# Kernel optimization log

Measured on AMD Instinct MI355X. Metric: run time of the kernel, lower is better.

The kernel has to match this reference:

```python
import jax, jax.numpy as jnp
import numpy as np

N = 10000      # nodes
E = 160000     # edges (before self-loops)
H = 2          # ATTN_HEADS
D_IN = 256
C1 = 256       # hidden_channels per head in conv1
C2 = 512       # per-head channels in conv2 (hardcoded 512 in module)
OUT = 3


def setup_inputs():
    key = jax.random.key(0)
    ks = jax.random.split(key, 20)
    rn = lambda k, s, sc=0.05: jax.random.normal(k, s, jnp.float32) * sc
    return {
        "x": jax.random.normal(ks[0], (N, D_IN), jnp.float32),
        "edge_index": jax.random.randint(ks[1], (2, E), 0, N),
        # conv1: lin_src/lin_dst [D_IN, H*C1], attention vecs [H, C1], bias [H*C1]
        "w1s": rn(ks[2], (D_IN, H * C1)), "w1d": rn(ks[3], (D_IN, H * C1)),
        "a1s": rn(ks[4], (H, C1)), "a1d": rn(ks[5], (H, C1)), "b1": rn(ks[6], (H * C1,)),
        # conv2: input dim H*C1 -> [H*C1, H*C2]
        "w2s": rn(ks[7], (H * C1, H * C2)), "w2d": rn(ks[8], (H * C1, H * C2)),
        "a2s": rn(ks[9], (H, C2)), "a2d": rn(ks[10], (H, C2)), "b2": rn(ks[11], (H * C2,)),
        # MLP head
        "wf1": rn(ks[12], (H * C2, 128)), "bf1": rn(ks[13], (128,)),
        "gamma": jnp.ones((128,), jnp.float32), "beta": jnp.zeros((128,), jnp.float32),
        "wf2": rn(ks[14], (128, OUT)), "bf2": rn(ks[15], (OUT,)),
    }


def gat_layer(x, src, dst, Ws, Wd, att_s, att_d, b, n):
    h, c = att_s.shape
    xs = (x @ Ws).reshape(n, h, c)                      # [N,H,C] source messages
    xd = (x @ Wd).reshape(n, h, c)
    a_s = (xs * att_s).sum(-1)                          # [N,H]
    a_d = (xd * att_d).sum(-1)
    e = a_s[src] + a_d[dst]                             # [E,H]
    e = jnp.where(e > 0, e, 0.2 * e)                    # leaky_relu(0.2)
    m = jax.lax.stop_gradient(jax.ops.segment_max(e, dst, num_segments=n))
    alpha = jnp.exp(e - m[dst])
    denom = jax.ops.segment_sum(alpha, dst, num_segments=n)
    alpha = alpha / denom[dst]                          # segment softmax over dst
    out = jax.ops.segment_sum(xs[src] * alpha[..., None], dst, num_segments=n)
    return out.reshape(n, h * c) + b                    # concat heads + bias


def reference(x, edge_index, w1s, w1d, a1s, a1d, b1, w2s, w2d, a2s, a2d, b2,
              wf1, bf1, gamma, beta, wf2, bf2):
    loops = jnp.arange(N, dtype=edge_index.dtype)
    src = jnp.concatenate([edge_index[0], loops])       # add self-loops (PyG default)
    dst = jnp.concatenate([edge_index[1], loops])
    h = jax.nn.relu(gat_layer(x, src, dst, w1s, w1d, a1s, a1d, b1, N))
    h = jax.nn.relu(gat_layer(h, src, dst, w2s, w2d, a2s, a2d, b2, N))
    h = h @ wf1 + bf1
    mean = h.mean(0)
    var = ((h - mean) ** 2).mean(0)
    h = gamma * (h - mean) * jax.lax.rsqrt(var + 1e-5) + beta
    h = jax.nn.relu(h)
    h = h @ wf2 + bf2
    return jax.nn.log_softmax(h, axis=-1)
```

## Files before the change

kernel.cpp:

```cpp
#include <hip/hip_runtime.h>
#include <cstdint>
#include <cstddef>


typedef unsigned short u16;
typedef __bf16 bf16x8 __attribute__((ext_vector_type(8)));
typedef float f32x4 __attribute__((ext_vector_type(4)));
typedef unsigned short u16x8 __attribute__((ext_vector_type(8)));

__device__ __forceinline__ u16 f2b(float f) {
  union { float f; uint32_t u; } c; c.f = f;
  uint32_t u = c.u;
  return (u16)((u + 0x7FFFu + ((u >> 16) & 1u)) >> 16);
}
__device__ __forceinline__ float b2f(u16 h) {
  union { uint32_t u; float f; } c; c.u = ((uint32_t)h) << 16;
  return c.f;
}

__device__ __forceinline__ void async16(const void* g, void* l) {
  __builtin_amdgcn_global_load_lds((const __attribute__((address_space(1))) void*)g,
                                   (__attribute__((address_space(3))) void*)l, 16, 0, 0);
}

__device__ __forceinline__ float2 edge_w(const float4& as, const float4& ad) {
  float e0 = as.x + ad.z; e0 = e0 > 0.f ? e0 : 0.2f * e0;
  float e1 = as.y + ad.w; e1 = e1 > 0.f ? e1 : 0.2f * e1;
  return make_float2(__expf(e0), __expf(e1));
}

__device__ __forceinline__ void transpose_tile(const float* __restrict__ W, u16* __restrict__ WT,
                                               int K, int NC, int b, int t,
                                               u16 (*tile)[66]) {
  int tn = NC >> 6;
  int ti = b / tn, tj = b - ti * tn;
  int col = t & 63, r0 = t >> 6;
  const float* src = W + (size_t)(ti * 64) * NC + tj * 64;
#pragma unroll
  for (int i = 0; i < 16; i++) {
    int r = r0 + i * 4;
    tile[r][col] = f2b(src[(size_t)r * NC + col]);
  }
  __syncthreads();
  u16* dst = WT + (size_t)(tj * 64) * K + ti * 64;
#pragma unroll
  for (int i = 0; i < 16; i++) {
    int r = r0 + i * 4;
    dst[(size_t)r * K + col] = tile[col][r];
  }
}

__global__ __launch_bounds__(256) void prep(
    const float* __restrict__ x,
    const float* __restrict__ w1s, const float* __restrict__ w1d,
    const float* __restrict__ w2s, const float* __restrict__ w2d,
    const float* __restrict__ wf1,
    const float* __restrict__ a1s, const float* __restrict__ a1d,
    const float* __restrict__ a2s, const float* __restrict__ a2d,
    u16* __restrict__ xb, u16* __restrict__ w1T, u16* __restrict__ w2T,
    u16* __restrict__ wf1T, float* __restrict__ V1, float* __restrict__ V2,
    uint32_t* __restrict__ arena, int arena_nwords, int za,
    uint32_t* __restrict__ g1pad, int g1w, int zg1,
    uint32_t* __restrict__ g2pad, int g2w,
    int N) {
  __shared__ u16 tile[64][66];
  int b = blockIdx.x, t = threadIdx.x;
  const int R0 = 32;
  const int R1 = R0 + 128;
  const int R2 = R1 + 32;
  const int R3 = R2 + 256;
  const int R4 = R3 + 512;
  const int R5 = R4 + N;
  const int R6 = R5 + za;
  const int R7 = R6 + zg1;

  if (b < R0) {
    transpose_tile(w1s, w1T, 256, 512, b, t, tile);
  } else if (b < R1) {
    transpose_tile(w2s, w2T, 512, 1024, b - R0, t, tile);
  } else if (b < R2) {
    transpose_tile(wf1, wf1T, 1024, 128, b - R1, t, tile);
  } else if (b < R3) {
    int wv = t >> 6, lane = t & 63;
    int u = (b - R2) * 4 + wv;
    int k = u >> 2, which = (u >> 1) & 1, h = u & 1;
    const float* W = which ? w1d : w1s;
    const float* att = which ? a1d : a1s;
    float s = 0.f;
#pragma unroll
    for (int c = lane; c < 256; c += 64) s += W[k * 512 + h * 256 + c] * att[h * 256 + c];
#pragma unroll
    for (int o = 32; o > 0; o >>= 1) s += __shfl_down(s, o);
    if (lane == 0) V1[k * 4 + which * 2 + h] = s;
  } else if (b < R4) {
    int wv = t >> 6, lane = t & 63;
    int u = (b - R3) * 4 + wv;
    int k = u >> 2, which = (u >> 1) & 1, h = u & 1;
    const float* W = which ? w2d : w2s;
    const float* att = which ? a2d : a2s;
    float s = 0.f;
#pragma unroll
    for (int c = lane; c < 512; c += 64) s += W[k * 1024 + h * 512 + c] * att[h * 512 + c];
#pragma unroll
    for (int o = 32; o > 0; o >>= 1) s += __shfl_down(s, o);
    if (lane == 0) V2[k * 4 + which * 2 + h] = s;
  } else if (b < R5) {
    int row = b - R4;
    int idx = row * 256 + t;
    xb[idx] = f2b(x[idx]);
  } else if (b < R6) {
    int idx = (b - R5) * 256 + t;
    if (idx < arena_nwords) arena[idx] = 0u;
  } else if (b < R7) {
    int idx = (b - R6) * 256 + t;
    if (idx < g1w) g1pad[idx] = 0u;
  } else {
    int idx = (b - R7) * 256 + t;
    if (idx < g2w) g2pad[idx] = 0u;
  }
}

__global__ __launch_bounds__(256) void fill_a(const int* __restrict__ srcs,
                                              const int* __restrict__ dsts,
                                              int* __restrict__ cursor, int* __restrict__ csr,
                                              const float* __restrict__ X,
                                              const float* __restrict__ V,
                                              float* __restrict__ A, int N, int E, int FB) {
  int b = blockIdx.x, t = threadIdx.x;
  if (b < FB) {
    int i = b * 256 + t;
    if (i < N) {
      csr[(size_t)i * 64] = i;
    } else if (i < N + E) {
      int e = i - N;
      int d = dsts[e];
      int slot = atomicAdd(&cursor[d], 1) + 1;
      if (slot < 64) csr[(size_t)d * 64 + slot] = srcs[e];
    }
    return;
  }
  int node = (b - FB) * 4 + (t >> 6);
  int lane = t & 63;
  if (node >= N) return;
  const float* xr = X + (size_t)node * 256;
  float s0 = 0, s1 = 0, s2 = 0, s3 = 0;
  {
    int k = lane * 4;
    float4 xv = *(const float4*)(xr + k);
    float xe[4] = {xv.x, xv.y, xv.z, xv.w};
#pragma unroll
    for (int j = 0; j < 4; j++) {
      float4 v = ((const float4*)V)[k + j];
      s0 += xe[j] * v.x; s1 += xe[j] * v.y; s2 += xe[j] * v.z; s3 += xe[j] * v.w;
    }
  }
#pragma unroll
  for (int o = 32; o > 0; o >>= 1) {
    s0 += __shfl_down(s0, o); s1 += __shfl_down(s1, o);
    s2 += __shfl_down(s2, o); s3 += __shfl_down(s3, o);
  }
  if (lane == 0) ((float4*)A)[node] = make_float4(s0, s1, s2, s3);
}

__global__ __launch_bounds__(256) void agg1(const u16* __restrict__ xs,
                                            const float* __restrict__ a,
                                            const int* __restrict__ cursor,
                                            const int* __restrict__ csr,
                                            u16* __restrict__ g, int N) {
  int v = blockIdx.x * 8 + (threadIdx.x >> 5);
  if (v >= N) return;
  int c0 = (threadIdx.x & 31) * 8;
  const int* seg = csr + (size_t)v * 64;
  int cnt = min(cursor[v], 63) + 1;
  const float4* a4 = (const float4*)a;
  float4 adv = a4[v];
  float h0[8], h1[8];
#pragma unroll
  for (int j = 0; j < 8; j++) { h0[j] = 0.f; h1[j] = 0.f; }
  float den0 = 0.f, den1 = 0.f;
  int i = 0;
  for (; i + 4 <= cnt; i += 4) {
    int4 s4 = *(const int4*)(seg + i);
    float4 aa0 = a4[s4.x], aa1 = a4[s4.y], aa2 = a4[s4.z], aa3 = a4[s4.w];
    u16x8 x0 = *(const u16x8*)(xs + (size_t)s4.x * 256 + c0);
    u16x8 x1 = *(const u16x8*)(xs + (size_t)s4.y * 256 + c0);
    u16x8 x2 = *(const u16x8*)(xs + (size_t)s4.z * 256 + c0);
    u16x8 x3 = *(const u16x8*)(xs + (size_t)s4.w * 256 + c0);
    float2 w0 = edge_w(aa0, adv), w1 = edge_w(aa1, adv);
    float2 w2 = edge_w(aa2, adv), w3 = edge_w(aa3, adv);
    den0 += w0.x + w1.x + w2.x + w3.x;
    den1 += w0.y + w1.y + w2.y + w3.y;
#pragma unroll
    for (int j = 0; j < 8; j++) {
      float f0 = b2f(x0[j]), f1 = b2f(x1[j]), f2 = b2f(x2[j]), f3 = b2f(x3[j]);
      h0[j] += w0.x * f0 + w1.x * f1 + w2.x * f2 + w3.x * f3;
      h1[j] += w0.y * f0 + w1.y * f1 + w2.y * f2 + w3.y * f3;
    }
  }
  for (; i < cnt; i++) {
    int s = seg[i];
    float2 w = edge_w(a4[s], adv);
    den0 += w.x; den1 += w.y;
    u16x8 xv = *(const u16x8*)(xs + (size_t)s * 256 + c0);
#pragma unroll
    for (int j = 0; j < 8; j++) {
      float f = b2f(xv[j]);
      h0[j] += w.x * f;
      h1[j] += w.y * f;
    }
  }
  float r0 = 1.f / den0, r1 = 1.f / den1;
  u16x8 o0v, o1v;
#pragma unroll
  for (int j = 0; j < 8; j++) {
    o0v[j] = f2b(h0[j] * r0);
    o1v[j] = f2b(h1[j] * r1);
  }
  u16* grow = g + (size_t)v * 512;
  *(u16x8*)(grow + c0) = o0v;
  *(u16x8*)(grow + 256 + c0) = o1v;
}

__global__ __launch_bounds__(256) void agg2(const u16* __restrict__ xs,
                                            const float* __restrict__ a,
                                            const int* __restrict__ cursor,
                                            const int* __restrict__ csr,
                                            u16* __restrict__ g, int N) {
  int v = blockIdx.x * 4 + (threadIdx.x >> 6);
  if (v >= N) return;
  int c0 = (threadIdx.x & 63) * 8;
  const int* seg = csr + (size_t)v * 64;
  int cnt = min(cursor[v], 63) + 1;
  const float4* a4 = (const float4*)a;
  float4 adv = a4[v];
  float h0[8], h1[8];
#pragma unroll
  for (int j = 0; j < 8; j++) { h0[j] = 0.f; h1[j] = 0.f; }
  float den0 = 0.f, den1 = 0.f;
  int i = 0;
  for (; i + 4 <= cnt; i += 4) {
    int4 s4 = *(const int4*)(seg + i);
    float4 aa0 = a4[s4.x], aa1 = a4[s4.y], aa2 = a4[s4.z], aa3 = a4[s4.w];
    u16x8 x0 = *(const u16x8*)(xs + (size_t)s4.x * 512 + c0);
    u16x8 x1 = *(const u16x8*)(xs + (size_t)s4.y * 512 + c0);
    u16x8 x2 = *(const u16x8*)(xs + (size_t)s4.z * 512 + c0);
    u16x8 x3 = *(const u16x8*)(xs + (size_t)s4.w * 512 + c0);
    float2 w0 = edge_w(aa0, adv), w1 = edge_w(aa1, adv);
    float2 w2 = edge_w(aa2, adv), w3 = edge_w(aa3, adv);
    den0 += w0.x + w1.x + w2.x + w3.x;
    den1 += w0.y + w1.y + w2.y + w3.y;
#pragma unroll
    for (int j = 0; j < 8; j++) {
      float f0 = b2f(x0[j]), f1 = b2f(x1[j]), f2 = b2f(x2[j]), f3 = b2f(x3[j]);
      h0[j] += w0.x * f0 + w1.x * f1 + w2.x * f2 + w3.x * f3;
      h1[j] += w0.y * f0 + w1.y * f1 + w2.y * f2 + w3.y * f3;
    }
  }
  for (; i < cnt; i++) {
    int s = seg[i];
    float2 w = edge_w(a4[s], adv);
    den0 += w.x; den1 += w.y;
    u16x8 xv = *(const u16x8*)(xs + (size_t)s * 512 + c0);
#pragma unroll
    for (int j = 0; j < 8; j++) {
      float f = b2f(xv[j]);
      h0[j] += w.x * f;
      h1[j] += w.y * f;
    }
  }
  float r0 = 1.f / den0, r1 = 1.f / den1;
  u16x8 o0v, o1v;
#pragma unroll
  for (int j = 0; j < 8; j++) {
    o0v[j] = f2b(h0[j] * r0);
    o1v[j] = f2b(h1[j] * r1);
  }
  u16* grow = g + (size_t)v * 1024;
  *(u16x8*)(grow + c0) = o0v;
  *(u16x8*)(grow + 512 + c0) = o1v;
}

template <bool OUT_BF16, bool A2OUT>
__global__ __launch_bounds__(256) void gemm_bf16(const u16* __restrict__ A, int lda, int aZ,
                                                 const u16* __restrict__ BT, int ldb, int bZ,
                                                 const float* __restrict__ bias, int biasZ,
                                                 int relu, void* __restrict__ Cv, int ldc,
                                                 size_t cZ, int K, float* __restrict__ a2out,
                                                 const float* __restrict__ Vfold) {
  __shared__ u16 Asl[2][128 * 32];
  __shared__ u16 Bsl[2][128 * 32];
  int tid = threadIdx.x;
  int wave = tid >> 6, lane = tid & 63;
  int wr = wave >> 1, wc = wave & 1;
  int lr = lane & 15, quad = lane >> 4;
  size_t row0 = (size_t)blockIdx.y * 128;
  size_t n0 = (size_t)blockIdx.x * 128;
  int zq = blockIdx.z;
  int k0base = 0;
  if (OUT_BF16) {
    A += (size_t)zq * aZ;
    BT += (size_t)zq * bZ;
    bias += (size_t)zq * biasZ;
  } else {
    k0base = zq * K;
  }

  f32x4 acc[4][4];
#pragma unroll
  for (int i = 0; i < 4; i++)
#pragma unroll
    for (int j = 0; j < 4; j++) acc[i][j] = (f32x4){0.f, 0.f, 0.f, 0.f};

  int ra = tid >> 2;
  int ca = (tid & 3) * 8;
  const u16* gA = A + (row0 + ra) * lda + ca;
  const u16* gB = BT + (n0 + ra) * ldb + ca;
  int lbase = (tid & 192) * 8;

  async16(gA + k0base, &Asl[0][lbase]);
  async16(gA + (size_t)64 * lda + k0base, &Asl[0][lbase + 2048]);
  async16(gB + k0base, &Bsl[0][lbase]);
  async16(gB + (size_t)64 * ldb + k0base, &Bsl[0][lbase + 2048]);
  __syncthreads();

  int nIter = K >> 5;
  for (int it = 0; it < nIter; it++) {
    int cur = it & 1;
    if (it + 1 < nIter) {
      int kn = k0base + (it + 1) * 32;
      async16(gA + kn, &Asl[1 - cur][lbase]);
      async16(gA + (size_t)64 * lda + kn, &Asl[1 - cur][lbase + 2048]);
      async16(gB + kn, &Bsl[1 - cur][lbase]);
      async16(gB + (size_t)64 * ldb + kn, &Bsl[1 - cur][lbase + 2048]);
    }
    bf16x8 av[4], bv[4];
#pragma unroll
    for (int i = 0; i < 4; i++)
      av[i] = *(const bf16x8*)&Asl[cur][(wr * 64 + i * 16 + lr) * 32 + quad * 8];
#pragma unroll
    for (int j = 0; j < 4; j++)
      bv[j] = *(const bf16x8*)&Bsl[cur][(wc * 64 + j * 16 + lr) * 32 + quad * 8];
#pragma unroll
    for (int i = 0; i < 4; i++)
#pragma unroll
      for (int j = 0; j < 4; j++)
        acc[i][j] = __builtin_amdgcn_mfma_f32_16x16x32_bf16(av[i], bv[j], acc[i][j], 0, 0, 0);
    __syncthreads();
  }

  size_t crow = row0 + wr * 64 + quad * 4;
  size_t ccol = n0 + wc * 64 + lr;
  if (OUT_BF16) {
    float bj[4];
#pragma unroll
    for (int j = 0; j < 4; j++) bj[j] = bias[ccol + j * 16];
    float4 vr[4];
    if (A2OUT) {
#pragma unroll
      for (int j = 0; j < 4; j++)
        vr[j] = ((const float4*)Vfold)[(size_t)zq * cZ + ccol + j * 16];
    }
    u16* C = (u16*)Cv + (size_t)zq * cZ;
#pragma unroll
    for (int i = 0; i < 4; i++) {
#pragma unroll
      for (int r = 0; r < 4; r++) {
        float pa0 = 0.f, pa1 = 0.f, pa2 = 0.f, pa3 = 0.f;
#pragma unroll
        for (int j = 0; j < 4; j++) {
          float val = acc[i][j][r] + bj[j];
          if (relu) val = fmaxf(val, 0.f);
          C[(crow + i * 16 + r) * ldc + ccol + j * 16] = f2b(val);
          if (A2OUT) {
            pa0 += val * vr[j].x; pa1 += val * vr[j].y;
            pa2 += val * vr[j].z; pa3 += val * vr[j].w;
          }
        }
        if (A2OUT) {
#pragma unroll
          for (int o = 8; o > 0; o >>= 1) {
            pa0 += __shfl_down(pa0, o); pa1 += __shfl_down(pa1, o);
            pa2 += __shfl_down(pa2, o); pa3 += __shfl_down(pa3, o);
          }
          if (lr == 0) {
            float* ap = a2out + (crow + i * 16 + r) * 4;
            atomicAdd(ap + 0, pa0); atomicAdd(ap + 1, pa1);
            atomicAdd(ap + 2, pa2); atomicAdd(ap + 3, pa3);
          }
        }
      }
    }
  } else {
    float* C = (float*)Cv + (size_t)zq * cZ;
#pragma unroll
    for (int i = 0; i < 4; i++)
#pragma unroll
      for (int j = 0; j < 4; j++)
#pragma unroll
        for (int r = 0; r < 4; r++)
          C[(crow + i * 16 + r) * ldc + ccol + j * 16] = acc[i][j][r];
  }
}

__global__ __launch_bounds__(128) void col_stats(const float* __restrict__ z, size_t slab,
                                                 float* __restrict__ sums, int N) {
  int j = threadIdx.x;
  float s = 0.f, s2 = 0.f;
  for (int n = blockIdx.x; n < N; n += gridDim.x) {
    const float* p = z + (size_t)n * 128 + j;
    float v = p[0] + p[slab] + p[2 * slab] + p[3 * slab];
    s += v; s2 += v * v;
  }
  atomicAdd(&sums[j], s);
  atomicAdd(&sums[128 + j], s2);
}

__global__ __launch_bounds__(256) void head_kernel(const float* __restrict__ z, size_t slab,
                                                   const float* __restrict__ sums,
                                                   const float* __restrict__ gamma,
                                                   const float* __restrict__ beta,
                                                   const float* __restrict__ wf2,
                                                   const float* __restrict__ bf2,
                                                   float* __restrict__ out, int N) {
  int v = blockIdx.x * 4 + (threadIdx.x >> 6);
  if (v >= N) return;
  int lane = threadIdx.x & 63;
  float inv = 1.f / (float)N;
  float p0 = 0.f, p1 = 0.f, p2 = 0.f;
#pragma unroll
  for (int half = 0; half < 2; half++) {
    int j = lane + half * 64;
    float mean = sums[j] * inv;
    float var = sums[128 + j] * inv - mean * mean;
    float rstd = rsqrtf(var + 1e-5f);
    const float* p = z + (size_t)v * 128 + j;
    float h = p[0] + p[slab] + p[2 * slab] + p[3 * slab];
    h = gamma[j] * (h - mean) * rstd + beta[j];
    h = h > 0.f ? h : 0.f;
    p0 += h * wf2[j * 3 + 0];
    p1 += h * wf2[j * 3 + 1];
    p2 += h * wf2[j * 3 + 2];
  }
#pragma unroll
  for (int o = 32; o > 0; o >>= 1) {
    p0 += __shfl_down(p0, o);
    p1 += __shfl_down(p1, o);
    p2 += __shfl_down(p2, o);
  }
  if (lane == 0) {
    float l0 = p0 + bf2[0], l1 = p1 + bf2[1], l2 = p2 + bf2[2];
    float mx = fmaxf(l0, fmaxf(l1, l2));
    float lse = mx + logf(__expf(l0 - mx) + __expf(l1 - mx) + __expf(l2 - mx));
    out[v * 3 + 0] = l0 - lse;
    out[v * 3 + 1] = l1 - lse;
    out[v * 3 + 2] = l2 - lse;
  }
}

extern "C" void kernel_launch(void* const* d_in, const int* in_sizes, int n_in,
                              void* d_out, int out_size, void* d_ws, size_t ws_size,
                              hipStream_t stream) {
  const float* x     = (const float*)d_in[0];
  const int*   ei    = (const int*)d_in[1];
  const float* w1s   = (const float*)d_in[2];
  const float* w1d   = (const float*)d_in[3];
  const float* a1s   = (const float*)d_in[4];
  const float* a1d   = (const float*)d_in[5];
  const float* b1    = (const float*)d_in[6];
  const float* w2s   = (const float*)d_in[7];
  const float* w2d   = (const float*)d_in[8];
  const float* a2s   = (const float*)d_in[9];
  const float* a2d   = (const float*)d_in[10];
  const float* b2    = (const float*)d_in[11];
  const float* wf1   = (const float*)d_in[12];
  const float* gamma = (const float*)d_in[14];
  const float* beta  = (const float*)d_in[15];
  const float* wf2   = (const float*)d_in[16];
  const float* bf2   = (const float*)d_in[17];
  float* out = (float*)d_out;

  const int N = in_sizes[0] / 256;
  const int E = in_sizes[1] / 2;
  const int Mpad = ((N + 127) / 128) * 128;
  (void)n_in; (void)out_size; (void)ws_size;

  char* ws = (char*)d_ws;
  size_t off = 0;
  auto alloc = [&](size_t bytes) -> char* {
    off = (off + 255) & ~(size_t)255;
    char* p = ws + off;
    off += bytes;
    return p;
  };
  u16* xb    = (u16*)alloc((size_t)N * 256 * 2);
  u16* w1T   = (u16*)alloc((size_t)512 * 256 * 2);
  u16* w2T   = (u16*)alloc((size_t)1024 * 512 * 2);
  u16* wf1T  = (u16*)alloc((size_t)128 * 1024 * 2);
  u16* g1    = (u16*)alloc((size_t)Mpad * 512 * 2);
  u16* h1    = (u16*)alloc((size_t)Mpad * 512 * 2);
  u16* g2    = (u16*)alloc((size_t)Mpad * 1024 * 2);
  u16* h2    = (u16*)alloc((size_t)Mpad * 1024 * 2);
  float* z   = (float*)alloc((size_t)4 * Mpad * 128 * 4);
  float* a1  = (float*)alloc((size_t)N * 16);
  float* V1  = (float*)alloc(256 * 16);
  float* V2  = (float*)alloc(512 * 16);
  int* csr   = (int*)alloc((size_t)N * 64 * 4);
  size_t curB = (size_t)N * 4;
  size_t a2B = (size_t)Mpad * 16;
  size_t arenaB = curB + a2B + 1024;
  char* arena = alloc(arenaB);
  int* cursor = (int*)arena;
  float* a2   = (float*)(arena + curB);
  float* sums = (float*)(arena + curB + a2B);

  int arena_nwords = (int)(arenaB / 4);
  int za  = (arena_nwords + 255) / 256;
  int g1w = (Mpad - N) * 512 * 2 / 4;
  int zg1 = (g1w + 255) / 256;
  int g2w = (Mpad - N) * 1024 * 2 / 4;
  int zg2 = (g2w + 255) / 256;
  int prep_blocks = 32 + 128 + 32 + 256 + 512 + N + za + zg1 + zg2;

  prep<<<prep_blocks, 256, 0, stream>>>(
      x, w1s, w1d, w2s, w2d, wf1, a1s, a1d, a2s, a2d,
      xb, w1T, w2T, wf1T, V1, V2,
      (uint32_t*)arena, arena_nwords, za,
      (uint32_t*)(g1 + (size_t)N * 512), g1w, zg1,
      (uint32_t*)(g2 + (size_t)N * 1024), g2w, N);

  const int* srcs = ei;
  const int* dsts = ei + E;

  int FB = (N + E + 255) / 256;
  fill_a<<<FB + (N + 3) / 4, 256, 0, stream>>>(srcs, dsts, cursor, csr, x, V1, a1, N, E, FB);

  int mt = Mpad / 128;
  size_t slab = (size_t)Mpad * 128;

  agg1<<<(N + 7) / 8, 256, 0, stream>>>(xb, a1, cursor, csr, g1, N);
  gemm_bf16<true, true><<<dim3(2, mt, 2), 256, 0, stream>>>(
      g1, 512, 256, w1T, 256, 256 * 256, b1, 256, 1, h1, 512, 256, 256, a2, V2);
  agg2<<<(N + 3) / 4, 256, 0, stream>>>(h1, a2, cursor, csr, g2, N);
  gemm_bf16<true, false><<<dim3(4, mt, 2), 256, 0, stream>>>(
      g2, 1024, 512, w2T, 512, 512 * 512, b2, 512, 1, h2, 1024, 512, 512, nullptr, nullptr);
  gemm_bf16<false, false><<<dim3(1, mt, 4), 256, 0, stream>>>(
      h2, 1024, 0, wf1T, 1024, 0, b2 , 0, 0, z, 128, slab, 256, nullptr, nullptr);
  col_stats<<<120, 128, 0, stream>>>(z, slab, sums, N);
  head_kernel<<<(N + 3) / 4, 256, 0, stream>>>(z, slab, sums, gamma, beta, wf2, bf2, out, N);
}
```

Before: 252.8 us.

## Fuse column stats into final GEMM, drop split-K, vectorize x bf16 cast

The final MLP GEMM no longer splits K into four z-slabs that later had to be summed. It runs the full K=1024 in one pass and computes per-column sum and sum-of-squares in its epilogue with wave shuffles and atomics. This removes the col_stats kernel, the slab reads in head_kernel and most of the z buffer. The cost is only 79 blocks for that GEMM (down from 316), so it has less parallelism. The x-to-bf16 conversion in prep is also vectorized with float4 loads and ushort4 stores, four rows per block.

```diff
diff --git a/kernel.cpp b/kernel.cpp
--- a/kernel.cpp
+++ b/kernel.cpp
@@ -70,7 +70,7 @@
   const int R2 = R1 + 32;
   const int R3 = R2 + 256;
   const int R4 = R3 + 512;
-  const int R5 = R4 + N;
+  const int R5 = R4 + N / 4;
   const int R6 = R5 + za;
   const int R7 = R6 + zg1;
 
@@ -105,9 +105,12 @@
     for (int o = 32; o > 0; o >>= 1) s += __shfl_down(s, o);
     if (lane == 0) V2[k * 4 + which * 2 + h] = s;
   } else if (b < R5) {
-    int row = b - R4;
-    int idx = row * 256 + t;
-    xb[idx] = f2b(x[idx]);
+    int r = (b - R4) * 4 + (t >> 6);
+    int c = (t & 63) * 4;
+    float4 xv = *(const float4*)(x + (size_t)r * 256 + c);
+    ushort4 st;
+    st.x = f2b(xv.x); st.y = f2b(xv.y); st.z = f2b(xv.z); st.w = f2b(xv.w);
+    *(ushort4*)(xb + (size_t)r * 256 + c) = st;
   } else if (b < R6) {
     int idx = (b - R5) * 256 + t;
     if (idx < arena_nwords) arena[idx] = 0u;
@@ -280,13 +283,14 @@
   *(u16x8*)(grow + 512 + c0) = o1v;
 }
 
-template <bool OUT_BF16, bool A2OUT>
+template <int OMODE, bool A2OUT>
 __global__ __launch_bounds__(256) void gemm_bf16(const u16* __restrict__ A, int lda, int aZ,
                                                  const u16* __restrict__ BT, int ldb, int bZ,
                                                  const float* __restrict__ bias, int biasZ,
                                                  int relu, void* __restrict__ Cv, int ldc,
                                                  size_t cZ, int K, float* __restrict__ a2out,
-                                                 const float* __restrict__ Vfold) {
+                                                 const float* __restrict__ Vfold,
+                                                 float* __restrict__ sums, int Nrows) {
   __shared__ u16 Asl[2][128 * 32];
   __shared__ u16 Bsl[2][128 * 32];
   int tid = threadIdx.x;
@@ -296,13 +300,10 @@
   size_t row0 = (size_t)blockIdx.y * 128;
   size_t n0 = (size_t)blockIdx.x * 128;
   int zq = blockIdx.z;
-  int k0base = 0;
-  if (OUT_BF16) {
+  if (OMODE == 1) {
     A += (size_t)zq * aZ;
     BT += (size_t)zq * bZ;
     bias += (size_t)zq * biasZ;
-  } else {
-    k0base = zq * K;
   }
 
   f32x4 acc[4][4];
@@ -317,17 +318,17 @@
   const u16* gB = BT + (n0 + ra) * ldb + ca;
   int lbase = (tid & 192) * 8;
 
-  async16(gA + k0base, &Asl[0][lbase]);
-  async16(gA + (size_t)64 * lda + k0base, &Asl[0][lbase + 2048]);
-  async16(gB + k0base, &Bsl[0][lbase]);
-  async16(gB + (size_t)64 * ldb + k0base, &Bsl[0][lbase + 2048]);
+  async16(gA, &Asl[0][lbase]);
+  async16(gA + (size_t)64 * lda, &Asl[0][lbase + 2048]);
+  async16(gB, &Bsl[0][lbase]);
+  async16(gB + (size_t)64 * ldb, &Bsl[0][lbase + 2048]);
   __syncthreads();
 
   int nIter = K >> 5;
   for (int it = 0; it < nIter; it++) {
     int cur = it & 1;
     if (it + 1 < nIter) {
-      int kn = k0base + (it + 1) * 32;
+      int kn = (it + 1) * 32;
       async16(gA + kn, &Asl[1 - cur][lbase]);
       async16(gA + (size_t)64 * lda + kn, &Asl[1 - cur][lbase + 2048]);
       async16(gB + kn, &Bsl[1 - cur][lbase]);
@@ -350,7 +351,7 @@
 
   size_t crow = row0 + wr * 64 + quad * 4;
   size_t ccol = n0 + wc * 64 + lr;
-  if (OUT_BF16) {
+  if (OMODE == 1) {
     float bj[4];
 #pragma unroll
     for (int j = 0; j < 4; j++) bj[j] = bias[ccol + j * 16];
@@ -391,31 +392,39 @@
       }
     }
   } else {
-    float* C = (float*)Cv + (size_t)zq * cZ;
+    float* C = (float*)Cv;
+    float s1[4] = {0.f, 0.f, 0.f, 0.f}, s2[4] = {0.f, 0.f, 0.f, 0.f};
 #pragma unroll
     for (int i = 0; i < 4; i++)
 #pragma unroll
-      for (int j = 0; j < 4; j++)
-#pragma unroll
-        for (int r = 0; r < 4; r++)
-          C[(crow + i * 16 + r) * ldc + ccol + j * 16] = acc[i][j][r];
-  }
-}
-
-__global__ __launch_bounds__(128) void col_stats(const float* __restrict__ z, size_t slab,
-                                                 float* __restrict__ sums, int N) {
-  int j = threadIdx.x;
-  float s = 0.f, s2 = 0.f;
-  for (int n = blockIdx.x; n < N; n += gridDim.x) {
-    const float* p = z + (size_t)n * 128 + j;
-    float v = p[0] + p[slab] + p[2 * slab] + p[3 * slab];
-    s += v; s2 += v * v;
-  }
-  atomicAdd(&sums[j], s);
-  atomicAdd(&sums[128 + j], s2);
-}
-
-__global__ __launch_bounds__(256) void head_kernel(const float* __restrict__ z, size_t slab,
+      for (int r = 0; r < 4; r++) {
+        size_t row = crow + i * 16 + r;
+#pragma unroll
+        for (int j = 0; j < 4; j++) {
+          float v = acc[i][j][r];
+          C[row * ldc + ccol + j * 16] = v;
+          if ((int)row < Nrows) { s1[j] += v; s2[j] += v * v; }
+        }
+      }
+#pragma unroll
+    for (int j = 0; j < 4; j++) {
+#pragma unroll
+      for (int o = 16; o < 64; o <<= 1) {
+        s1[j] += __shfl_down(s1[j], o);
+        s2[j] += __shfl_down(s2[j], o);
+      }
+    }
+    if (quad == 0) {
+#pragma unroll
+      for (int j = 0; j < 4; j++) {
+        atomicAdd(&sums[ccol + j * 16], s1[j]);
+        atomicAdd(&sums[128 + ccol + j * 16], s2[j]);
+      }
+    }
+  }
+}
+
+__global__ __launch_bounds__(256) void head_kernel(const float* __restrict__ z,
                                                    const float* __restrict__ sums,
                                                    const float* __restrict__ gamma,
                                                    const float* __restrict__ beta,
@@ -433,8 +442,7 @@
     float mean = sums[j] * inv;
     float var = sums[128 + j] * inv - mean * mean;
     float rstd = rsqrtf(var + 1e-5f);
-    const float* p = z + (size_t)v * 128 + j;
-    float h = p[0] + p[slab] + p[2 * slab] + p[3 * slab];
+    float h = z[(size_t)v * 128 + j];
     h = gamma[j] * (h - mean) * rstd + beta[j];
     h = h > 0.f ? h : 0.f;
     p0 += h * wf2[j * 3 + 0];
@@ -500,7 +508,7 @@
   u16* h1    = (u16*)alloc((size_t)Mpad * 512 * 2);
   u16* g2    = (u16*)alloc((size_t)Mpad * 1024 * 2);
   u16* h2    = (u16*)alloc((size_t)Mpad * 1024 * 2);
-  float* z   = (float*)alloc((size_t)4 * Mpad * 128 * 4);
+  float* z   = (float*)alloc((size_t)Mpad * 128 * 4);
   float* a1  = (float*)alloc((size_t)N * 16);
   float* V1  = (float*)alloc(256 * 16);
   float* V2  = (float*)alloc(512 * 16);
@@ -519,7 +527,7 @@
   int zg1 = (g1w + 255) / 256;
   int g2w = (Mpad - N) * 1024 * 2 / 4;
   int zg2 = (g2w + 255) / 256;
-  int prep_blocks = 32 + 128 + 32 + 256 + 512 + N + za + zg1 + zg2;
+  int prep_blocks = 32 + 128 + 32 + 256 + 512 + N / 4 + za + zg1 + zg2;
 
   prep<<<prep_blocks, 256, 0, stream>>>(
       x, w1s, w1d, w2s, w2d, wf1, a1s, a1d, a2s, a2d,
@@ -535,16 +543,17 @@
   fill_a<<<FB + (N + 3) / 4, 256, 0, stream>>>(srcs, dsts, cursor, csr, x, V1, a1, N, E, FB);
 
   int mt = Mpad / 128;
-  size_t slab = (size_t)Mpad * 128;
 
   agg1<<<(N + 7) / 8, 256, 0, stream>>>(xb, a1, cursor, csr, g1, N);
-  gemm_bf16<true, true><<<dim3(2, mt, 2), 256, 0, stream>>>(
-      g1, 512, 256, w1T, 256, 256 * 256, b1, 256, 1, h1, 512, 256, 256, a2, V2);
+  gemm_bf16<1, true><<<dim3(2, mt, 2), 256, 0, stream>>>(
+      g1, 512, 256, w1T, 256, 256 * 256, b1, 256, 1, h1, 512, 256, 256, a2, V2,
+      nullptr, 0);
   agg2<<<(N + 3) / 4, 256, 0, stream>>>(h1, a2, cursor, csr, g2, N);
-  gemm_bf16<true, false><<<dim3(4, mt, 2), 256, 0, stream>>>(
-      g2, 1024, 512, w2T, 512, 512 * 512, b2, 512, 1, h2, 1024, 512, 512, nullptr, nullptr);
-  gemm_bf16<false, false><<<dim3(1, mt, 4), 256, 0, stream>>>(
-      h2, 1024, 0, wf1T, 1024, 0, b2 , 0, 0, z, 128, slab, 256, nullptr, nullptr);
-  col_stats<<<120, 128, 0, stream>>>(z, slab, sums, N);
-  head_kernel<<<(N + 3) / 4, 256, 0, stream>>>(z, slab, sums, gamma, beta, wf2, bf2, out, N);
-}
+  gemm_bf16<1, false><<<dim3(4, mt, 2), 256, 0, stream>>>(
+      g2, 1024, 512, w2T, 512, 512 * 512, b2, 512, 1, h2, 1024, 512, 512, nullptr, nullptr,
+      nullptr, 0);
+  gemm_bf16<0, false><<<dim3(1, mt, 1), 256, 0, stream>>>(
+      h2, 1024, 0, wf1T, 1024, 0, b2 , 0, 0, z, 128, 0, 1024, nullptr, nullptr,
+      sums, N);
+  head_kernel<<<(N + 3) / 4, 256, 0, stream>>>(z, sums, gamma, beta, wf2, bf2, out, N);
+}
```

Result: faster. 232.9 us (-7.9%).
